# Optimization experiments

Hardware: AMD Instinct MI355X
Metric: run time of the kernel (lower is better)

The kernel has to match this reference:

```python
import jax, jax.numpy as jnp
import numpy as np

B, FH, FW, T = 128, 26, 26, 50
A, NUM_CLASSES = 5, 20
IGNORE_THRESH = 0.75
COORD_SCALE, NOOBJ_SCALE, OBJ_SCALE, CLASS_SCALE = 1.0, 1.0, 5.0, 1.0
ANCHORS = jnp.array([[1.3221, 1.73145], [3.19275, 4.00944], [5.05587, 8.09892],
                     [9.47112, 4.84053], [11.2364, 10.0071]], dtype=jnp.float32)


def xywh2xxyy(b):
    return jnp.stack([b[:, 0] - b[:, 2] / 2, b[:, 1] - b[:, 3] / 2,
                      b[:, 0] + b[:, 2] / 2, b[:, 1] + b[:, 3] / 2], axis=1)


def xxyy2xywh(b):
    return jnp.stack([(b[:, 0] + b[:, 2]) / 2, (b[:, 1] + b[:, 3]) / 2,
                      b[:, 2] - b[:, 0], b[:, 3] - b[:, 1]], axis=1)


def pair_iou(b1, b2):
    # b1: [N,4] xxyy, b2: [K,4] xxyy -> [N,K]
    xi1 = jnp.maximum(b1[:, None, 0], b2[None, :, 0])
    yi1 = jnp.maximum(b1[:, None, 1], b2[None, :, 1])
    xi2 = jnp.minimum(b1[:, None, 2], b2[None, :, 2])
    yi2 = jnp.minimum(b1[:, None, 3], b2[None, :, 3])
    inter = jnp.maximum(xi2 - xi1, 0.0) * jnp.maximum(yi2 - yi1, 0.0)
    a1 = ((b1[:, 2] - b1[:, 0]) * (b1[:, 3] - b1[:, 1]))[:, None]
    a2 = ((b2[:, 2] - b2[:, 0]) * (b2[:, 3] - b2[:, 1]))[None, :]
    return inter / (a1 + a2 - inter)


def make_all_anchors(F_H, F_W):
    ys, xs = jnp.meshgrid(jnp.arange(F_H), jnp.arange(F_W), indexing='ij')
    cells = jnp.stack([xs.ravel(), ys.ravel()], axis=-1).astype(jnp.float32)  # [K,2] (c_x, c_y)
    K = F_H * F_W
    all_anch = jnp.concatenate([jnp.broadcast_to(cells[:, None, :], (K, A, 2)),
                                jnp.broadcast_to(ANCHORS[None, :, :], (K, A, 2))], axis=-1)
    return all_anch.reshape(K * A, 4)  # (c_x, c_y, p_w, p_h), top-left-cell coords


def _build_target_single(box_deltas, gt, all_anch, anch_xxyy, F_H, F_W):
    # box_deltas: [K*A,4] (sig tx, sig ty, exp tw, exp th); gt: [T,5]
    K = F_H * F_W
    valid = gt[:, :4].sum(-1) > 0
    scale = jnp.array([F_W, F_H, F_W, F_H], dtype=jnp.float32)
    gt_xxyy = gt[:, :4] * scale  # [T,4] grid units
    # predicted boxes
    pred = jnp.stack([all_anch[:, 0] + box_deltas[:, 0], all_anch[:, 1] + box_deltas[:, 1],
                      all_anch[:, 2] * box_deltas[:, 2], all_anch[:, 3] * box_deltas[:, 3]], axis=1)
    pred_xxyy = xywh2xxyy(pred)
    ious = pair_iou(pred_xxyy, gt_xxyy)                       # [K*A, T]
    ious = jnp.where(valid[None, :], ious, -1.0)
    max_iou = ious.max(axis=-1)                               # [K*A]
    pos_any = jnp.any(max_iou > IGNORE_THRESH)
    iou_mask0 = jnp.where(pos_any & (max_iou >= IGNORE_THRESH), 0.0, NOOBJ_SCALE).reshape(K, A)
    # anchor-gt overlaps for responsibility assignment
    overlaps = pair_iou(anch_xxyy, gt_xxyy).reshape(K, A, T)
    gt_xcycwh = xxyy2xywh(gt_xxyy)                            # [T,4]
    cx = jnp.clip(jnp.floor(gt_xcycwh[:, 0]).astype(jnp.int32), 0, F_W - 1)
    cy = jnp.clip(jnp.floor(gt_xcycwh[:, 1]).astype(jnp.int32), 0, F_H - 1)
    cell = cy * F_W + cx                                      # [T]
    aidx = jnp.argmax(overlaps[cell, :, jnp.arange(T)], axis=-1)  # [T]
    anch_ka = all_anch.reshape(K, A, 4)
    assigned = anch_ka[cell, aidx]                            # [T,4]
    tgt_box = jnp.stack([gt_xcycwh[:, 0] - assigned[:, 0], gt_xcycwh[:, 1] - assigned[:, 1],
                         gt_xcycwh[:, 2] / assigned[:, 2], gt_xcycwh[:, 3] / assigned[:, 3]], axis=1)
    miou_t = max_iou.reshape(K, A)[cell, aidx]                # [T]
    cls_t = gt[:, 4]
    carry0 = (jnp.zeros((K, A)), iou_mask0, jnp.zeros((K, A, 4)),
              jnp.zeros((K, A)), jnp.zeros((K, A)), jnp.zeros((K, A)))
    def step(c, xs):
        it, im, bt, bm, ct, cm = c
        ce, an, v, tb, cl, mi = xs
        def w(arr, new):
            return arr.at[ce, an].set(jnp.where(v, new, arr[ce, an]))
        return (w(it, mi), w(im, OBJ_SCALE), w(bt, tb), w(bm, 1.0), w(ct, cl), w(cm, 1.0)), None
    (it, im, bt, bm, ct, cm), _ = jax.lax.scan(step, carry0, (cell, aidx, valid, tgt_box, cls_t, miou_t))
    return it, im, bt, bm, ct, cm


def setup_inputs() -> dict:
    key = jax.random.key(0)
    k1, k2, k3, k4, k5 = jax.random.split(key, 5)
    outputs = jax.random.normal(k1, (B, A * (5 + NUM_CLASSES), FH, FW), dtype=jnp.float32) * 0.1
    x1 = jax.random.uniform(k2, (B, T, 1), minval=0.02, maxval=0.75)
    y1 = jax.random.uniform(k3, (B, T, 1), minval=0.02, maxval=0.75)
    wh = jax.random.uniform(k4, (B, T, 2), minval=0.05, maxval=0.2)
    cls = jax.random.randint(k5, (B, T, 1), 0, NUM_CLASSES).astype(jnp.float32)
    targets = jnp.concatenate([x1, y1, x1 + wh[..., :1], y1 + wh[..., 1:]], axis=-1)
    targets = jnp.concatenate([targets, cls], axis=-1)  # [B, T, 5]
    return {"outputs": outputs, "targets": targets}


def reference(outputs, targets):
    Bn, _, F_H, F_W = outputs.shape
    out = outputs.transpose(0, 2, 3, 1).reshape(Bn, F_H * F_W * A, 5 + NUM_CLASSES)
    xy = jax.nn.sigmoid(out[..., 0:2])
    wh = jnp.exp(out[..., 2:4])
    conf = jax.nn.sigmoid(out[..., 4])            # [B, K*A]
    cls_score = out[..., 5:]                      # [B, K*A, C]
    box_delta = jnp.concatenate([xy, wh], axis=-1)  # [B, K*A, 4]
    all_anch = make_all_anchors(F_H, F_W)
    anch_xcycwh = all_anch.at[:, :2].add(0.5)
    anch_xxyy = xywh2xxyy(anch_xcycwh)
    it, im, bt, bm, ct, cm = jax.vmap(
        lambda d, g: _build_target_single(d, g, all_anch, anch_xxyy, F_H, F_W))(box_delta, targets)
    it = it.reshape(Bn, -1)
    im = im.reshape(Bn, -1)
    bt = bt.reshape(Bn, -1, 4)
    bm = bm.reshape(Bn, -1, 1)
    ct = ct.reshape(Bn, -1).astype(jnp.int32)
    cm = cm.reshape(Bn, -1)
    box_loss = COORD_SCALE * jnp.sum((box_delta * bm - bt * bm) ** 2) / 2.0 / Bn
    iou_loss = jnp.sum((conf * im - it * im) ** 2) / 2.0 / Bn
    logp = jax.nn.log_softmax(cls_score, axis=-1)
    ce = -jnp.take_along_axis(logp, ct[..., None], axis=-1)[..., 0]
    class_loss = CLASS_SCALE * jnp.sum(cm * ce) / Bn
    return box_loss + iou_loss + class_loss
```

## Files before the change

kernel.cpp:

```cpp
#include <hip/hip_runtime.h>
#include <math.h>

constexpr int BN = 128;
constexpr int FH = 26, FW = 26;
constexpr int T  = 50;
constexpr int A  = 5;
constexpr int NC = 20;
constexpr int K  = FH * FW;
constexpr int KA = K * A;
constexpr int CH = A * (5 + NC);

constexpr float IGNORE_THRESH = 0.75f;
constexpr float OBJ_SCALE = 5.0f;

constexpr int CHUNKS = (KA + 255) / 256;
constexpr int NPART  = BN * CHUNKS;

__constant__ float ANCW[A] = {1.3221f, 3.19275f, 5.05587f, 9.47112f, 11.2364f};
__constant__ float ANCH[A] = {1.73145f, 4.00944f, 8.09892f, 4.84053f, 10.0071f};

__device__ __forceinline__ float fast_sigmoid(float x) {
    return __builtin_amdgcn_rcpf(1.0f + __expf(-x));
}

__global__ __launch_bounds__(256) void yolo_main(
        const float* __restrict__ outputs,
        const float* __restrict__ targets,
        float* __restrict__ Lp, float* __restrict__ Mp, int* __restrict__ Anyp) {
    __shared__ float4 sbox[T];
    __shared__ float2 sas[T];
    __shared__ float4 stb[T];
    __shared__ float  scls[T];
    __shared__ float  redl[4], redm[4];
    __shared__ int    reda[4];

    const int b   = blockIdx.y;
    const int tid = threadIdx.x;

    if (tid < T) {
        const float* g = targets + ((size_t)b * T + tid) * 5;
        float rx1 = g[0], ry1 = g[1], rx2 = g[2], ry2 = g[3];
        bool valid = (rx1 + ry1 + rx2 + ry2) > 0.0f;
        float x1 = rx1 * FW, y1 = ry1 * FH, x2 = rx2 * FW, y2 = ry2 * FH;
        float w = x2 - x1, h = y2 - y1;

        float cxf = 0.5f * (x1 + x2), cyf = 0.5f * (y1 + y2);
        int cx = (int)floorf(cxf); cx = min(max(cx, 0), FW - 1);
        int cy = (int)floorf(cyf); cy = min(max(cy, 0), FH - 1);
        int cell = cy * FW + cx;

        float acx = (float)cx + 0.5f, acy = (float)cy + 0.5f;
        float best = -1.0f; int ai = 0;
        for (int a = 0; a < A; ++a) {
            float aw = ANCW[a], ah = ANCH[a];
            float xi1 = fmaxf(acx - 0.5f * aw, x1), yi1 = fmaxf(acy - 0.5f * ah, y1);
            float xi2 = fminf(acx + 0.5f * aw, x2), yi2 = fminf(acy + 0.5f * ah, y2);
            float inter = fmaxf(xi2 - xi1, 0.0f) * fmaxf(yi2 - yi1, 0.0f);
            float iou = inter / (aw * ah + w * h - inter);
            if (iou > best) { best = iou; ai = a; }
        }

        if (valid) {
            sbox[tid] = make_float4(x1, y1, x2, y2);
            sas[tid]  = make_float2(w * h, __int_as_float(ai * K + cell));
        } else {
            sbox[tid] = make_float4(1e18f, 1e18f, -1e18f, -1e18f);
            sas[tid]  = make_float2(1.0f, __int_as_float(-1));
        }
        stb[tid]  = make_float4(cxf - (float)cx, cyf - (float)cy,
                                w / ANCW[ai], h / ANCH[ai]);
        scls[tid] = g[4];
    }
    __syncthreads();

    const int s = blockIdx.x * 256 + tid;
    float loss = 0.0f, masked = 0.0f;
    int any = 0;

    if (s < KA) {
        const int a = s / K, k = s - a * K;
        const int y = k / FW, x = k - y * FW;
        const float* ob = outputs + (size_t)b * CH * K;

        float o0 = ob[(a * 25 + 0) * K + k];
        float o1 = ob[(a * 25 + 1) * K + k];
        float o2 = ob[(a * 25 + 2) * K + k];
        float o3 = ob[(a * 25 + 3) * K + k];
        float o4 = ob[(a * 25 + 4) * K + k];

        float s0 = fast_sigmoid(o0), s1 = fast_sigmoid(o1);
        float e2 = __expf(o2),       e3 = __expf(o3);
        float px = (float)x + s0, py = (float)y + s1;
        float pw = ANCW[a] * e2,  ph = ANCH[a] * e3;
        float px1 = px - 0.5f * pw, px2 = px + 0.5f * pw;
        float py1 = py - 0.5f * ph, py2 = py + 0.5f * ph;
        float parea = pw * ph;

        float m = -1.0f;
        int w = -1;
        #pragma unroll 10
        for (int t = 0; t < T; ++t) {
            float4 bx  = sbox[t];
            float2 as2 = sas[t];
            float xi1 = fmaxf(px1, bx.x), yi1 = fmaxf(py1, bx.y);
            float xi2 = fminf(px2, bx.z), yi2 = fminf(py2, bx.w);
            float iw = fmaxf(xi2 - xi1, 0.0f), ih = fmaxf(yi2 - yi1, 0.0f);
            float inter = iw * ih;
            float iou = inter * __builtin_amdgcn_rcpf(parea + as2.x - inter);
            m = fmaxf(m, iou);
            if (__float_as_int(as2.y) == s) w = t;
        }
        any = (m > IGNORE_THRESH) ? 1 : 0;

        float conf = fast_sigmoid(o4);
        if (w >= 0) {
            float d = (conf - m) * OBJ_SCALE;
            loss += 0.5f * d * d;
            float4 tb = stb[w];
            float d0 = s0 - tb.x, d1 = s1 - tb.y;
            float d2 = e2 - tb.z, d3 = e3 - tb.w;
            loss += 0.5f * (d0 * d0 + d1 * d1 + d2 * d2 + d3 * d3);

            float v[NC];
            #pragma unroll
            for (int c = 0; c < NC; ++c) v[c] = ob[(a * 25 + 5 + c) * K + k];
            float mx = v[0];
            #pragma unroll
            for (int c = 1; c < NC; ++c) mx = fmaxf(mx, v[c]);
            float se = 0.0f;
            #pragma unroll
            for (int c = 0; c < NC; ++c) se += __expf(v[c] - mx);
            int cls = (int)scls[w];
            loss += (__logf(se) + mx) - v[cls];
        } else {
            float term = 0.5f * conf * conf;
            loss += term;
            if (m >= IGNORE_THRESH) masked += term;
        }
    }

    for (int off = 32; off > 0; off >>= 1) {
        loss   += __shfl_down(loss, off);
        masked += __shfl_down(masked, off);
    }
    any = __any(any) ? 1 : 0;
    int lane = tid & 63, wv = tid >> 6;
    if (lane == 0) { redl[wv] = loss; redm[wv] = masked; reda[wv] = any; }
    __syncthreads();
    if (tid == 0) {
        int idx = b * CHUNKS + blockIdx.x;
        Lp[idx]   = redl[0] + redl[1] + redl[2] + redl[3];
        Mp[idx]   = redm[0] + redm[1] + redm[2] + redm[3];
        Anyp[idx] = reda[0] | reda[1] | reda[2] | reda[3];
    }
}

__global__ __launch_bounds__(128) void yolo_fix(
        const float* __restrict__ Lp, const float* __restrict__ Mp,
        const int* __restrict__ Anyp, float* __restrict__ out) {
    __shared__ float red[2];
    int tid = threadIdx.x;
    float L = 0.0f, M = 0.0f;
    int any = 0;
    if (tid < BN) {
        #pragma unroll
        for (int c = 0; c < CHUNKS; ++c) {
            int idx = tid * CHUNKS + c;
            L += Lp[idx];
            M += Mp[idx];
            any |= Anyp[idx];
        }
    }
    float acc = L - (any ? M : 0.0f);
    for (int off = 32; off > 0; off >>= 1) acc += __shfl_down(acc, off);
    if ((tid & 63) == 0) red[tid >> 6] = acc;
    __syncthreads();
    if (tid == 0) out[0] = (red[0] + red[1]) * (1.0f / (float)BN);
}

extern "C" void kernel_launch(void* const* d_in, const int* in_sizes, int n_in,
                              void* d_out, int out_size, void* d_ws, size_t ws_size,
                              hipStream_t stream) {
    const float* outputs = (const float*)d_in[0];
    const float* targets = (const float*)d_in[1];
    float* out = (float*)d_out;

    float* Lp   = (float*)d_ws;
    float* Mp   = Lp + NPART;
    int*   Anyp = (int*)(Mp + NPART);

    yolo_main<<<dim3(CHUNKS, BN), 256, 0, stream>>>(outputs, targets, Lp, Mp, Anyp);
    yolo_fix<<<1, 128, 0, stream>>>(Lp, Mp, Anyp, out);
}
```

Baseline: 93.00 us.

## Process four anchor slots per thread with float4 loads and shared box reads

```diff
diff --git a/kernel.cpp b/kernel.cpp
--- a/kernel.cpp
+++ b/kernel.cpp
@@ -13,8 +13,9 @@
 constexpr float IGNORE_THRESH = 0.75f;
 constexpr float OBJ_SCALE = 5.0f;
 
-constexpr int CHUNKS = (KA + 255) / 256;
-constexpr int NPART  = BN * CHUNKS;
+constexpr int NG      = KA / 4;
+constexpr int GCHUNKS = (NG + 255) / 256;
+constexpr int NPART   = BN * GCHUNKS;
 
 __constant__ float ANCW[A] = {1.3221f, 3.19275f, 5.05587f, 9.47112f, 11.2364f};
 __constant__ float ANCH[A] = {1.73145f, 4.00944f, 8.09892f, 4.84053f, 10.0071f};
@@ -37,9 +38,24 @@
     const int b   = blockIdx.y;
     const int tid = threadIdx.x;
 
+    const int g      = blockIdx.x * 256 + tid;
+    const bool live  = g < NG;
+    const int a      = live ? (g / 169) : 0;
+    const int k0     = (g - a * 169) * 4;
+    const float* ob  = outputs + (size_t)b * CH * K + (size_t)(a * 25) * K;
+
+    float4 o0, o1, o2, o3, o4;
+    if (live) {
+        o0 = *(const float4*)(ob + 0 * K + k0);
+        o1 = *(const float4*)(ob + 1 * K + k0);
+        o2 = *(const float4*)(ob + 2 * K + k0);
+        o3 = *(const float4*)(ob + 3 * K + k0);
+        o4 = *(const float4*)(ob + 4 * K + k0);
+    }
+
     if (tid < T) {
-        const float* g = targets + ((size_t)b * T + tid) * 5;
-        float rx1 = g[0], ry1 = g[1], rx2 = g[2], ry2 = g[3];
+        const float* gt = targets + ((size_t)b * T + tid) * 5;
+        float rx1 = gt[0], ry1 = gt[1], rx2 = gt[2], ry2 = gt[3];
         bool valid = (rx1 + ry1 + rx2 + ry2) > 0.0f;
         float x1 = rx1 * FW, y1 = ry1 * FH, x2 = rx2 * FW, y2 = ry2 * FH;
         float w = x2 - x1, h = y2 - y1;
@@ -51,13 +67,13 @@
 
         float acx = (float)cx + 0.5f, acy = (float)cy + 0.5f;
         float best = -1.0f; int ai = 0;
-        for (int a = 0; a < A; ++a) {
-            float aw = ANCW[a], ah = ANCH[a];
+        for (int aa = 0; aa < A; ++aa) {
+            float aw = ANCW[aa], ah = ANCH[aa];
             float xi1 = fmaxf(acx - 0.5f * aw, x1), yi1 = fmaxf(acy - 0.5f * ah, y1);
             float xi2 = fminf(acx + 0.5f * aw, x2), yi2 = fminf(acy + 0.5f * ah, y2);
             float inter = fmaxf(xi2 - xi1, 0.0f) * fmaxf(yi2 - yi1, 0.0f);
             float iou = inter / (aw * ah + w * h - inter);
-            if (iou > best) { best = iou; ai = a; }
+            if (iou > best) { best = iou; ai = aa; }
         }
 
         if (valid) {
@@ -69,73 +85,88 @@
         }
         stb[tid]  = make_float4(cxf - (float)cx, cyf - (float)cy,
                                 w / ANCW[ai], h / ANCH[ai]);
-        scls[tid] = g[4];
+        scls[tid] = gt[4];
     }
     __syncthreads();
 
-    const int s = blockIdx.x * 256 + tid;
     float loss = 0.0f, masked = 0.0f;
-    int any = 0;
-
-    if (s < KA) {
-        const int a = s / K, k = s - a * K;
-        const int y = k / FW, x = k - y * FW;
-        const float* ob = outputs + (size_t)b * CH * K;
-
-        float o0 = ob[(a * 25 + 0) * K + k];
-        float o1 = ob[(a * 25 + 1) * K + k];
-        float o2 = ob[(a * 25 + 2) * K + k];
-        float o3 = ob[(a * 25 + 3) * K + k];
-        float o4 = ob[(a * 25 + 4) * K + k];
-
-        float s0 = fast_sigmoid(o0), s1 = fast_sigmoid(o1);
-        float e2 = __expf(o2),       e3 = __expf(o3);
-        float px = (float)x + s0, py = (float)y + s1;
-        float pw = ANCW[a] * e2,  ph = ANCH[a] * e3;
-        float px1 = px - 0.5f * pw, px2 = px + 0.5f * pw;
-        float py1 = py - 0.5f * ph, py2 = py + 0.5f * ph;
-        float parea = pw * ph;
-
-        float m = -1.0f;
-        int w = -1;
-        #pragma unroll 10
+    int anyf = 0;
+
+    if (live) {
+        const int s0 = a * K + k0;
+        const float oo0[4] = {o0.x, o0.y, o0.z, o0.w};
+        const float oo1[4] = {o1.x, o1.y, o1.z, o1.w};
+        const float oo2[4] = {o2.x, o2.y, o2.z, o2.w};
+        const float oo3[4] = {o3.x, o3.y, o3.z, o3.w};
+        const float oo4[4] = {o4.x, o4.y, o4.z, o4.w};
+
+        float s0v[4], s1v[4], e2v[4], e3v[4];
+        float px1[4], px2[4], py1[4], py2[4], parea[4], mm[4];
+        int   wi[4];
+        #pragma unroll
+        for (int j = 0; j < 4; ++j) {
+            int k = k0 + j;
+            int yy = k / FW, xx = k - yy * FW;
+            s0v[j] = fast_sigmoid(oo0[j]);
+            s1v[j] = fast_sigmoid(oo1[j]);
+            e2v[j] = __expf(oo2[j]);
+            e3v[j] = __expf(oo3[j]);
+            float px = (float)xx + s0v[j], py = (float)yy + s1v[j];
+            float pw = ANCW[a] * e2v[j],  ph = ANCH[a] * e3v[j];
+            px1[j] = px - 0.5f * pw; px2[j] = px + 0.5f * pw;
+            py1[j] = py - 0.5f * ph; py2[j] = py + 0.5f * ph;
+            parea[j] = pw * ph;
+            mm[j] = -1.0f;
+            wi[j] = -1;
+        }
+
+        #pragma unroll 5
         for (int t = 0; t < T; ++t) {
             float4 bx  = sbox[t];
             float2 as2 = sas[t];
-            float xi1 = fmaxf(px1, bx.x), yi1 = fmaxf(py1, bx.y);
-            float xi2 = fminf(px2, bx.z), yi2 = fminf(py2, bx.w);
-            float iw = fmaxf(xi2 - xi1, 0.0f), ih = fmaxf(yi2 - yi1, 0.0f);
-            float inter = iw * ih;
-            float iou = inter * __builtin_amdgcn_rcpf(parea + as2.x - inter);
-            m = fmaxf(m, iou);
-            if (__float_as_int(as2.y) == s) w = t;
-        }
-        any = (m > IGNORE_THRESH) ? 1 : 0;
-
-        float conf = fast_sigmoid(o4);
-        if (w >= 0) {
-            float d = (conf - m) * OBJ_SCALE;
-            loss += 0.5f * d * d;
-            float4 tb = stb[w];
-            float d0 = s0 - tb.x, d1 = s1 - tb.y;
-            float d2 = e2 - tb.z, d3 = e3 - tb.w;
-            loss += 0.5f * (d0 * d0 + d1 * d1 + d2 * d2 + d3 * d3);
-
-            float v[NC];
+            int slot_t = __float_as_int(as2.y);
             #pragma unroll
-            for (int c = 0; c < NC; ++c) v[c] = ob[(a * 25 + 5 + c) * K + k];
-            float mx = v[0];
-            #pragma unroll
-            for (int c = 1; c < NC; ++c) mx = fmaxf(mx, v[c]);
-            float se = 0.0f;
-            #pragma unroll
-            for (int c = 0; c < NC; ++c) se += __expf(v[c] - mx);
-            int cls = (int)scls[w];
-            loss += (__logf(se) + mx) - v[cls];
-        } else {
-            float term = 0.5f * conf * conf;
-            loss += term;
-            if (m >= IGNORE_THRESH) masked += term;
+            for (int j = 0; j < 4; ++j) {
+                float xi1 = fmaxf(px1[j], bx.x), yi1 = fmaxf(py1[j], bx.y);
+                float xi2 = fminf(px2[j], bx.z), yi2 = fminf(py2[j], bx.w);
+                float iw = fmaxf(xi2 - xi1, 0.0f), ih = fmaxf(yi2 - yi1, 0.0f);
+                float inter = iw * ih;
+                float iou = inter * __builtin_amdgcn_rcpf(parea[j] + as2.x - inter);
+                mm[j] = fmaxf(mm[j], iou);
+                if (slot_t == s0 + j) wi[j] = t;
+            }
+        }
+
+        #pragma unroll
+        for (int j = 0; j < 4; ++j) {
+            float m = mm[j];
+            anyf |= (m > IGNORE_THRESH) ? 1 : 0;
+            float conf = fast_sigmoid(oo4[j]);
+            int w = wi[j];
+            if (w >= 0) {
+                float d = (conf - m) * OBJ_SCALE;
+                loss += 0.5f * d * d;
+                float4 tb = stb[w];
+                float d0 = s0v[j] - tb.x, d1 = s1v[j] - tb.y;
+                float d2 = e2v[j] - tb.z, d3 = e3v[j] - tb.w;
+                loss += 0.5f * (d0 * d0 + d1 * d1 + d2 * d2 + d3 * d3);
+
+                float v[NC];
+                #pragma unroll
+                for (int c = 0; c < NC; ++c) v[c] = ob[(5 + c) * K + k0 + j];
+                float mx = v[0];
+                #pragma unroll
+                for (int c = 1; c < NC; ++c) mx = fmaxf(mx, v[c]);
+                float se = 0.0f;
+                #pragma unroll
+                for (int c = 0; c < NC; ++c) se += __expf(v[c] - mx);
+                int cls = (int)scls[w];
+                loss += (__logf(se) + mx) - v[cls];
+            } else {
+                float term = 0.5f * conf * conf;
+                loss += term;
+                if (m >= IGNORE_THRESH) masked += term;
+            }
         }
     }
 
@@ -143,12 +174,12 @@
         loss   += __shfl_down(loss, off);
         masked += __shfl_down(masked, off);
     }
-    any = __any(any) ? 1 : 0;
+    anyf = __any(anyf) ? 1 : 0;
     int lane = tid & 63, wv = tid >> 6;
-    if (lane == 0) { redl[wv] = loss; redm[wv] = masked; reda[wv] = any; }
+    if (lane == 0) { redl[wv] = loss; redm[wv] = masked; reda[wv] = anyf; }
     __syncthreads();
     if (tid == 0) {
-        int idx = b * CHUNKS + blockIdx.x;
+        int idx = b * GCHUNKS + blockIdx.x;
         Lp[idx]   = redl[0] + redl[1] + redl[2] + redl[3];
         Mp[idx]   = redm[0] + redm[1] + redm[2] + redm[3];
         Anyp[idx] = reda[0] | reda[1] | reda[2] | reda[3];
@@ -164,8 +195,8 @@
     int any = 0;
     if (tid < BN) {
         #pragma unroll
-        for (int c = 0; c < CHUNKS; ++c) {
-            int idx = tid * CHUNKS + c;
+        for (int c = 0; c < GCHUNKS; ++c) {
+            int idx = tid * GCHUNKS + c;
             L += Lp[idx];
             M += Mp[idx];
             any |= Anyp[idx];
@@ -189,6 +220,6 @@
     float* Mp   = Lp + NPART;
     int*   Anyp = (int*)(Mp + NPART);
 
-    yolo_main<<<dim3(CHUNKS, BN), 256, 0, stream>>>(outputs, targets, Lp, Mp, Anyp);
+    yolo_main<<<dim3(GCHUNKS, BN), 256, 0, stream>>>(outputs, targets, Lp, Mp, Anyp);
     yolo_fix<<<1, 128, 0, stream>>>(Lp, Mp, Anyp, out);
 }
```

New measurement: 97.43 us. +4.8%, slower.

## Precompute GT box data in a prep kernel and fuse final reduction via atomic counter

Applied to the files above, without the earlier changes.

```diff
diff --git a/kernel.cpp b/kernel.cpp
--- a/kernel.cpp
+++ b/kernel.cpp
@@ -13,8 +13,8 @@
 constexpr float IGNORE_THRESH = 0.75f;
 constexpr float OBJ_SCALE = 5.0f;
 
-constexpr int CHUNKS = (KA + 255) / 256;
-constexpr int NPART  = BN * CHUNKS;
+constexpr int GCH  = (KA + 255) / 256;
+constexpr int NBLK = BN * GCH;
 
 __constant__ float ANCW[A] = {1.3221f, 3.19275f, 5.05587f, 9.47112f, 11.2364f};
 __constant__ float ANCH[A] = {1.73145f, 4.00944f, 8.09892f, 4.84053f, 10.0071f};
@@ -23,70 +23,78 @@
     return __builtin_amdgcn_rcpf(1.0f + __expf(-x));
 }
 
+__global__ __launch_bounds__(256) void yolo_prep(
+        const float* __restrict__ targets,
+        float* __restrict__ giou, float* __restrict__ gtb,
+        unsigned* __restrict__ cnt) {
+    int i = blockIdx.x * 256 + threadIdx.x;
+    if (i == 0) *cnt = 0u;
+    if (i >= BN * T) return;
+
+    const float* g = targets + (size_t)i * 5;
+    float rx1 = g[0], ry1 = g[1], rx2 = g[2], ry2 = g[3];
+    bool valid = (rx1 + ry1 + rx2 + ry2) > 0.0f;
+    float x1 = rx1 * FW, y1 = ry1 * FH, x2 = rx2 * FW, y2 = ry2 * FH;
+    float w = x2 - x1, h = y2 - y1;
+
+    float cxf = 0.5f * (x1 + x2), cyf = 0.5f * (y1 + y2);
+    int cx = (int)floorf(cxf); cx = min(max(cx, 0), FW - 1);
+    int cy = (int)floorf(cyf); cy = min(max(cy, 0), FH - 1);
+    int cell = cy * FW + cx;
+
+    float acx = (float)cx + 0.5f, acy = (float)cy + 0.5f;
+    float best = -1.0f; int ai = 0;
+    for (int a = 0; a < A; ++a) {
+        float aw = ANCW[a], ah = ANCH[a];
+        float xi1 = fmaxf(acx - 0.5f * aw, x1), yi1 = fmaxf(acy - 0.5f * ah, y1);
+        float xi2 = fminf(acx + 0.5f * aw, x2), yi2 = fminf(acy + 0.5f * ah, y2);
+        float inter = fmaxf(xi2 - xi1, 0.0f) * fmaxf(yi2 - yi1, 0.0f);
+        float iou = inter / (aw * ah + w * h - inter);
+        if (iou > best) { best = iou; ai = a; }
+    }
+
+    float4 p0, p1;
+    if (valid) {
+        p0 = make_float4(x1, y1, x2, y2);
+        p1 = make_float4(w * h, __int_as_float(ai * K + cell), 0.0f, 0.0f);
+    } else {
+        p0 = make_float4(1e18f, 1e18f, -1e18f, -1e18f);
+        p1 = make_float4(1.0f, __int_as_float(-1), 0.0f, 0.0f);
+    }
+    *(float4*)(giou + (size_t)i * 8)     = p0;
+    *(float4*)(giou + (size_t)i * 8 + 4) = p1;
+    *(float4*)(gtb  + (size_t)i * 8)     = make_float4(cxf - (float)cx, cyf - (float)cy,
+                                                       w / ANCW[ai], h / ANCH[ai]);
+    *(float4*)(gtb  + (size_t)i * 8 + 4) = make_float4(g[4], 0.0f, 0.0f, 0.0f);
+}
+
 __global__ __launch_bounds__(256) void yolo_main(
         const float* __restrict__ outputs,
-        const float* __restrict__ targets,
-        float* __restrict__ Lp, float* __restrict__ Mp, int* __restrict__ Anyp) {
-    __shared__ float4 sbox[T];
-    __shared__ float2 sas[T];
-    __shared__ float4 stb[T];
-    __shared__ float  scls[T];
-    __shared__ float  redl[4], redm[4];
-    __shared__ int    reda[4];
+        const float* __restrict__ giou, const float* __restrict__ gtb,
+        float* __restrict__ Lp, float* __restrict__ Mp, int* __restrict__ Anyp,
+        unsigned* __restrict__ cnt, float* __restrict__ out) {
+    __shared__ float redl[4], redm[4];
+    __shared__ int   reda[4];
+    __shared__ int   lastFlag;
 
     const int b   = blockIdx.y;
     const int tid = threadIdx.x;
-
-    if (tid < T) {
-        const float* g = targets + ((size_t)b * T + tid) * 5;
-        float rx1 = g[0], ry1 = g[1], rx2 = g[2], ry2 = g[3];
-        bool valid = (rx1 + ry1 + rx2 + ry2) > 0.0f;
-        float x1 = rx1 * FW, y1 = ry1 * FH, x2 = rx2 * FW, y2 = ry2 * FH;
-        float w = x2 - x1, h = y2 - y1;
-
-        float cxf = 0.5f * (x1 + x2), cyf = 0.5f * (y1 + y2);
-        int cx = (int)floorf(cxf); cx = min(max(cx, 0), FW - 1);
-        int cy = (int)floorf(cyf); cy = min(max(cy, 0), FH - 1);
-        int cell = cy * FW + cx;
-
-        float acx = (float)cx + 0.5f, acy = (float)cy + 0.5f;
-        float best = -1.0f; int ai = 0;
-        for (int a = 0; a < A; ++a) {
-            float aw = ANCW[a], ah = ANCH[a];
-            float xi1 = fmaxf(acx - 0.5f * aw, x1), yi1 = fmaxf(acy - 0.5f * ah, y1);
-            float xi2 = fminf(acx + 0.5f * aw, x2), yi2 = fminf(acy + 0.5f * ah, y2);
-            float inter = fmaxf(xi2 - xi1, 0.0f) * fmaxf(yi2 - yi1, 0.0f);
-            float iou = inter / (aw * ah + w * h - inter);
-            if (iou > best) { best = iou; ai = a; }
-        }
-
-        if (valid) {
-            sbox[tid] = make_float4(x1, y1, x2, y2);
-            sas[tid]  = make_float2(w * h, __int_as_float(ai * K + cell));
-        } else {
-            sbox[tid] = make_float4(1e18f, 1e18f, -1e18f, -1e18f);
-            sas[tid]  = make_float2(1.0f, __int_as_float(-1));
-        }
-        stb[tid]  = make_float4(cxf - (float)cx, cyf - (float)cy,
-                                w / ANCW[ai], h / ANCH[ai]);
-        scls[tid] = g[4];
-    }
-    __syncthreads();
-
-    const int s = blockIdx.x * 256 + tid;
+    const int s   = blockIdx.x * 256 + tid;
+    const bool live = s < KA;
+
     float loss = 0.0f, masked = 0.0f;
-    int any = 0;
-
-    if (s < KA) {
+    int anyf = 0;
+
+    if (live) {
         const int a = s / K, k = s - a * K;
         const int y = k / FW, x = k - y * FW;
-        const float* ob = outputs + (size_t)b * CH * K;
-
-        float o0 = ob[(a * 25 + 0) * K + k];
-        float o1 = ob[(a * 25 + 1) * K + k];
-        float o2 = ob[(a * 25 + 2) * K + k];
-        float o3 = ob[(a * 25 + 3) * K + k];
-        float o4 = ob[(a * 25 + 4) * K + k];
+        const float* ob = outputs + (size_t)b * CH * K + (size_t)(a * 25) * K;
+
+        float o0 = ob[0 * K + k];
+        float o1 = ob[1 * K + k];
+        float o2 = ob[2 * K + k];
+        float o3 = ob[3 * K + k];
+        float o4 = ob[4 * K + k];
 
         float s0 = fast_sigmoid(o0), s1 = fast_sigmoid(o1);
         float e2 = __expf(o2),       e3 = __expf(o3);
@@ -96,41 +104,45 @@
         float py1 = py - 0.5f * ph, py2 = py + 0.5f * ph;
         float parea = pw * ph;
 
+        const float* gb = giou + (size_t)b * T * 8;
+
         float m = -1.0f;
         int w = -1;
         #pragma unroll 10
         for (int t = 0; t < T; ++t) {
-            float4 bx  = sbox[t];
-            float2 as2 = sas[t];
-            float xi1 = fmaxf(px1, bx.x), yi1 = fmaxf(py1, bx.y);
-            float xi2 = fminf(px2, bx.z), yi2 = fminf(py2, bx.w);
+            float bx1 = gb[t * 8 + 0], by1 = gb[t * 8 + 1];
+            float bx2 = gb[t * 8 + 2], by2 = gb[t * 8 + 3];
+            float area = gb[t * 8 + 4];
+            int slot_t = __float_as_int(gb[t * 8 + 5]);
+            float xi1 = fmaxf(px1, bx1), yi1 = fmaxf(py1, by1);
+            float xi2 = fminf(px2, bx2), yi2 = fminf(py2, by2);
             float iw = fmaxf(xi2 - xi1, 0.0f), ih = fmaxf(yi2 - yi1, 0.0f);
             float inter = iw * ih;
-            float iou = inter * __builtin_amdgcn_rcpf(parea + as2.x - inter);
+            float iou = inter * __builtin_amdgcn_rcpf(parea + area - inter);
             m = fmaxf(m, iou);
-            if (__float_as_int(as2.y) == s) w = t;
+            if (slot_t == s) w = t;
         }
-        any = (m > IGNORE_THRESH) ? 1 : 0;
+        anyf = (m > IGNORE_THRESH) ? 1 : 0;
 
         float conf = fast_sigmoid(o4);
         if (w >= 0) {
             float d = (conf - m) * OBJ_SCALE;
             loss += 0.5f * d * d;
-            float4 tb = stb[w];
-            float d0 = s0 - tb.x, d1 = s1 - tb.y;
-            float d2 = e2 - tb.z, d3 = e3 - tb.w;
+            const float* tb = gtb + ((size_t)b * T + w) * 8;
+            float d0 = s0 - tb[0], d1 = s1 - tb[1];
+            float d2 = e2 - tb[2], d3 = e3 - tb[3];
             loss += 0.5f * (d0 * d0 + d1 * d1 + d2 * d2 + d3 * d3);
 
             float v[NC];
             #pragma unroll
-            for (int c = 0; c < NC; ++c) v[c] = ob[(a * 25 + 5 + c) * K + k];
+            for (int c = 0; c < NC; ++c) v[c] = ob[(5 + c) * K + k];
             float mx = v[0];
             #pragma unroll
             for (int c = 1; c < NC; ++c) mx = fmaxf(mx, v[c]);
             float se = 0.0f;
             #pragma unroll
             for (int c = 0; c < NC; ++c) se += __expf(v[c] - mx);
-            int cls = (int)scls[w];
+            int cls = (int)tb[4];
             loss += (__logf(se) + mx) - v[cls];
         } else {
             float term = 0.5f * conf * conf;
@@ -143,39 +155,42 @@
         loss   += __shfl_down(loss, off);
         masked += __shfl_down(masked, off);
     }
-    any = __any(any) ? 1 : 0;
+    anyf = __any(anyf) ? 1 : 0;
     int lane = tid & 63, wv = tid >> 6;
-    if (lane == 0) { redl[wv] = loss; redm[wv] = masked; reda[wv] = any; }
+    if (lane == 0) { redl[wv] = loss; redm[wv] = masked; reda[wv] = anyf; }
     __syncthreads();
     if (tid == 0) {
-        int idx = b * CHUNKS + blockIdx.x;
+        int idx = b * GCH + blockIdx.x;
         Lp[idx]   = redl[0] + redl[1] + redl[2] + redl[3];
         Mp[idx]   = redm[0] + redm[1] + redm[2] + redm[3];
         Anyp[idx] = reda[0] | reda[1] | reda[2] | reda[3];
-    }
-}
-
-__global__ __launch_bounds__(128) void yolo_fix(
-        const float* __restrict__ Lp, const float* __restrict__ Mp,
-        const int* __restrict__ Anyp, float* __restrict__ out) {
-    __shared__ float red[2];
-    int tid = threadIdx.x;
-    float L = 0.0f, M = 0.0f;
-    int any = 0;
-    if (tid < BN) {
-        #pragma unroll
-        for (int c = 0; c < CHUNKS; ++c) {
-            int idx = tid * CHUNKS + c;
-            L += Lp[idx];
-            M += Mp[idx];
-            any |= Anyp[idx];
+        __threadfence();
+        unsigned old = atomicAdd(cnt, 1u);
+        lastFlag = (old == (unsigned)(NBLK - 1));
+    }
+    __syncthreads();
+
+    if (lastFlag) {
+        __threadfence();
+        float acc = 0.0f;
+        if (tid < BN) {
+            float L = 0.0f, M = 0.0f;
+            int any = 0;
+            #pragma unroll
+            for (int c = 0; c < GCH; ++c) {
+                int idx = tid * GCH + c;
+                L += Lp[idx];
+                M += Mp[idx];
+                any |= Anyp[idx];
+            }
+            acc = L - (any ? M : 0.0f);
         }
-    }
-    float acc = L - (any ? M : 0.0f);
-    for (int off = 32; off > 0; off >>= 1) acc += __shfl_down(acc, off);
-    if ((tid & 63) == 0) red[tid >> 6] = acc;
-    __syncthreads();
-    if (tid == 0) out[0] = (red[0] + red[1]) * (1.0f / (float)BN);
+        for (int off = 32; off > 0; off >>= 1) acc += __shfl_down(acc, off);
+        if (lane == 0) redl[wv] = acc;
+        __syncthreads();
+        if (tid == 0)
+            out[0] = (redl[0] + redl[1] + redl[2] + redl[3]) * (1.0f / (float)BN);
+    }
 }
 
 extern "C" void kernel_launch(void* const* d_in, const int* in_sizes, int n_in,
@@ -185,10 +200,14 @@
     const float* targets = (const float*)d_in[1];
     float* out = (float*)d_out;
 
-    float* Lp   = (float*)d_ws;
-    float* Mp   = Lp + NPART;
-    int*   Anyp = (int*)(Mp + NPART);
-
-    yolo_main<<<dim3(CHUNKS, BN), 256, 0, stream>>>(outputs, targets, Lp, Mp, Anyp);
-    yolo_fix<<<1, 128, 0, stream>>>(Lp, Mp, Anyp, out);
-}
+    float*    giou = (float*)d_ws;
+    float*    gtb  = giou + (size_t)BN * T * 8;
+    float*    Lp   = gtb + (size_t)BN * T * 8;
+    float*    Mp   = Lp + NBLK;
+    int*      Anyp = (int*)(Mp + NBLK);
+    unsigned* cnt  = (unsigned*)(Anyp + NBLK);
+
+    yolo_prep<<<(BN * T + 255) / 256, 256, 0, stream>>>(targets, giou, gtb, cnt);
+    yolo_main<<<dim3(GCH, BN), 256, 0, stream>>>(outputs, giou, gtb,
+                                                 Lp, Mp, Anyp, cnt, out);
+}
```

Measured after the change: 135.7 us. 1.46x slower.
